# Kernel tuning notes

Hardware: AMD Instinct MI355X
Metric: run time of the kernel (lower is better)

The kernel has to match this reference:

```python
import jax, jax.numpy as jnp
import numpy as np

B, S, D, H = 2, 2048, 2048, 16
NEG = -1e9


def setup_inputs() -> dict:
    key = jax.random.key(0)
    ks = jax.random.split(key, 5)
    x = jax.random.normal(ks[0], (B, S, D), dtype=jnp.float32)
    # additive causal mask: 0 on/below diagonal, -1e9 above
    causal = jnp.triu(jnp.full((S, S), NEG, dtype=jnp.float32), k=1)
    attn_mask = causal[None, None, :, :]  # [1,1,S,S]
    scale = 0.02
    Wq = jax.random.normal(ks[1], (D, D), dtype=jnp.float32) * scale
    Wk = jax.random.normal(ks[2], (D, D), dtype=jnp.float32) * scale
    Wv = jax.random.normal(ks[3], (D, D), dtype=jnp.float32) * scale
    Wo = jax.random.normal(ks[4], (D, D), dtype=jnp.float32) * scale
    return {"x": x, "attn_mask": attn_mask, "Wq": Wq, "Wk": Wk, "Wv": Wv, "Wo": Wo}


def reference(x, attn_mask, Wq, Wk, Wv, Wo):
    b, s, hidden = x.shape
    d = hidden // H
    # torch nn.Linear: y = x @ W.T (no bias since bias=None)
    q = (x @ Wq.T).reshape(b, s, H, d).transpose(0, 2, 1, 3)  # [b,h,s,d]
    k = (x @ Wk.T).reshape(b, s, H, d).transpose(0, 2, 1, 3)
    v = (x @ Wv.T).reshape(b, s, H, d).transpose(0, 2, 1, 3)
    q = q * (1.0 / float(d) ** 0.5)
    att = jnp.einsum("bhqd,bhkd->bhqk", q, k) + attn_mask  # [b,h,s,s]
    att = jax.nn.softmax(att.astype(jnp.float32), axis=-1).astype(x.dtype)
    y = jnp.einsum("bhqk,bhkd->bhqd", att, v)
    y = y.transpose(0, 2, 1, 3).reshape(b, s, hidden)
    return y @ Wo.T
```

## Files before the change

kernel.cpp:

```cpp
#include <hip/hip_runtime.h>
#include <hip/hip_bf16.h>
#include <cstdint>
#include <cstddef>

typedef __bf16 bf16;
typedef __bf16 bf16x8 __attribute__((ext_vector_type(8)));
typedef __bf16 bf16x4 __attribute__((ext_vector_type(4)));
typedef float f32x4 __attribute__((ext_vector_type(4)));

static constexpr int BATCH = 2;
static constexpr int SEQ = 2048;
static constexpr int DMODEL = 2048;
static constexpr int NH = 16;
static constexpr int HD = 128;
static constexpr int MROWS = BATCH * SEQ;

#define GLOBAL_AS(p) ((const __attribute__((address_space(1))) void*)(p))
#define LDS_AS(p)    ((__attribute__((address_space(3))) void*)(p))

__global__ void cvt5_kernel(const float* __restrict__ x,
                            const float* __restrict__ wq, const float* __restrict__ wk,
                            const float* __restrict__ wv, const float* __restrict__ wo,
                            bf16* __restrict__ dst) {
  const int i = blockIdx.x * blockDim.x + threadIdx.x;
  const float* src;
  int local;
  if (i < 2097152) { src = x; local = i; }
  else {
    const int r = i - 2097152;
    const int w = r >> 20;
    local = r & 1048575;
    src = (w == 0) ? wq : (w == 1) ? wk : (w == 2) ? wv : wo;
  }
  float4 f = reinterpret_cast<const float4*>(src)[local];
  bf16x4 o;
  o.x = (bf16)f.x; o.y = (bf16)f.y; o.z = (bf16)f.z; o.w = (bf16)f.w;
  reinterpret_cast<bf16x4*>(dst)[i] = o;
}

enum { MODE_QKV = 0, MODE_OUT = 1 };

template <int MODE>
__global__ __launch_bounds__(256, 4) void gemm_bt(
    const bf16* __restrict__ A, const bf16* __restrict__ W,
    bf16* __restrict__ Oq, bf16* __restrict__ Ok, bf16* __restrict__ Ov,
    float* __restrict__ Oout) {
  constexpr int Kd = DMODEL;
  __shared__ __align__(16) bf16 As[128][64];
  __shared__ __align__(16) bf16 Bs[128][64];
  const int n0 = blockIdx.x * 128;
  const int m0 = blockIdx.y * 128;
  const int tid = threadIdx.x;
  const int wave = tid >> 6;
  const int lane = tid & 63;
  const int quad = lane >> 4;
  const int l16 = lane & 15;
  const int wm = (wave >> 1) * 64;
  const int wn = (wave & 1) * 64;
  const int srow = lane >> 3;
  const int schunk = ((lane & 7) - srow) & 7;

  f32x4 acc[4][4] = {};
  for (int kt = 0; kt < Kd; kt += 64) {
#pragma unroll
    for (int i = 0; i < 4; i++) {
      const int r = wave * 32 + i * 8;
      __builtin_amdgcn_global_load_lds(
          GLOBAL_AS(&A[(size_t)(m0 + r + srow) * Kd + kt + schunk * 8]),
          LDS_AS(&As[r][0]), 16, 0, 0);
      __builtin_amdgcn_global_load_lds(
          GLOBAL_AS(&W[(size_t)(n0 + r + srow) * Kd + kt + schunk * 8]),
          LDS_AS(&Bs[r][0]), 16, 0, 0);
    }
    __syncthreads();
#pragma unroll
    for (int ks = 0; ks < 2; ks++) {
      const int col = (((ks * 4 + quad + l16) & 7)) * 8;
      bf16x8 af[4], bfr[4];
#pragma unroll
      for (int t = 0; t < 4; t++)
        af[t] = *reinterpret_cast<const bf16x8*>(&As[wm + t * 16 + l16][col]);
#pragma unroll
      for (int t = 0; t < 4; t++)
        bfr[t] = *reinterpret_cast<const bf16x8*>(&Bs[wn + t * 16 + l16][col]);
#pragma unroll
      for (int tm = 0; tm < 4; tm++)
#pragma unroll
        for (int tn = 0; tn < 4; tn++)
          acc[tm][tn] = __builtin_amdgcn_mfma_f32_16x16x32_bf16(af[tm], bfr[tn], acc[tm][tn], 0, 0, 0);
    }
    __syncthreads();
  }
#pragma unroll
  for (int tm = 0; tm < 4; tm++) {
#pragma unroll
    for (int tn = 0; tn < 4; tn++) {
      const int row0 = m0 + wm + tm * 16 + quad * 4;
      if constexpr (MODE == MODE_OUT) {
        const int col = n0 + wn + tn * 16 + l16;
#pragma unroll
        for (int j = 0; j < 4; j++)
          Oout[(size_t)(row0 + j) * DMODEL + col] = acc[tm][tn][j];
      } else {
        const int mat = n0 >> 11;
        const int col = (n0 & 2047) + wn + tn * 16 + l16;
        const int h = col >> 7, dd = col & 127;
        if (mat == 2) {
          const int b = row0 >> 11, s = row0 & 2047;
          bf16x4 pk;
#pragma unroll
          for (int j = 0; j < 4; j++) pk[j] = (bf16)acc[tm][tn][j];
          *reinterpret_cast<bf16x4*>(&Ov[((size_t)(b * NH + h) * HD + dd) * SEQ + s]) = pk;
        } else {
          bf16* O = mat ? Ok : Oq;
          const float scale = mat ? 1.0f : 0.08838834764831845f;
#pragma unroll
          for (int j = 0; j < 4; j++) {
            const int row = row0 + j;
            const int b = row >> 11, s = row & 2047;
            O[((size_t)(b * NH + h) * SEQ + s) * HD + dd] = (bf16)(acc[tm][tn][j] * scale);
          }
        }
      }
    }
  }
}

__global__ __launch_bounds__(256, 2) void attn_kernel(
    const bf16* __restrict__ Q, const bf16* __restrict__ K,
    const bf16* __restrict__ Vt, bf16* __restrict__ Y) {
  const int j = blockIdx.x;
  const int bh = blockIdx.y;
  __shared__ __align__(16) char smem[54528];
  auto Ks  = (bf16(*)[128])smem;
  auto Vts = (bf16(*)[64])(smem + 16384);
  auto Ps  = (bf16(*)[16][72])(smem + 32768);
  const int tid = threadIdx.x;
  const int wave = tid >> 6;
  const int lane = tid & 63;
  const int quad = lane >> 4;
  const int l16 = lane & 15;

  const bf16* Kbh = K + (size_t)bh * SEQ * HD;
  const bf16* Vbh = Vt + (size_t)bh * HD * SEQ;
  const int b = bh >> 4, h = bh & 15;

  const int krow = lane >> 4;
  const int vrow = lane >> 3;
  const int vchunk = ((lane & 7) - vrow) & 7;

  for (int pass = 0; pass < 2; ++pass) {
    const int qt = pass ? (31 - j) : j;
    const int q0 = qt * 64;
    const int ntiles = qt + 1;

    const bf16* Qw = Q + ((size_t)bh * SEQ + q0 + wave * 16) * HD;
    bf16x8 qf[4];
#pragma unroll
    for (int kk = 0; kk < 4; kk++)
      qf[kk] = *reinterpret_cast<const bf16x8*>(&Qw[(size_t)l16 * HD + kk * 32 + quad * 8]);

    f32x4 oacc[8] = {};
    float m_i = -3.0e38f, l_i = 0.f;

    for (int t = 0; t < ntiles; ++t) {
      const int kt = t * 64;
#pragma unroll
      for (int i = 0; i < 4; i++) {
        const int rbase = wave * 16 + i * 4;
        const int r = rbase + krow;
        const int c = ((lane & 15) - krow - i * 4) & 15;
        __builtin_amdgcn_global_load_lds(
            GLOBAL_AS(&Kbh[(size_t)(kt + r) * HD + c * 8]), LDS_AS(&Ks[rbase][0]), 16, 0, 0);
      }
#pragma unroll
      for (int i = 0; i < 4; i++) {
        const int rbase = wave * 32 + i * 8;
        const int r = rbase + vrow;
        __builtin_amdgcn_global_load_lds(
            GLOBAL_AS(&Vbh[(size_t)r * SEQ + kt + vchunk * 8]), LDS_AS(&Vts[rbase][0]), 16, 0, 0);
      }
      __syncthreads();

      f32x4 sacc[4] = {};
#pragma unroll
      for (int kk = 0; kk < 4; kk++) {
        const int kcol = (((kk * 4 + quad + l16) & 15)) * 8;
        bf16x8 ka[4];
#pragma unroll
        for (int mt = 0; mt < 4; mt++)
          ka[mt] = *reinterpret_cast<const bf16x8*>(&Ks[mt * 16 + l16][kcol]);
#pragma unroll
        for (int mt = 0; mt < 4; mt++)
          sacc[mt] = __builtin_amdgcn_mfma_f32_16x16x32_bf16(ka[mt], qf[kk], sacc[mt], 0, 0, 0);
      }

      const int qg_loc = wave * 16 + l16;
      float mx = -3.0e38f;
      if (t == ntiles - 1) {
#pragma unroll
        for (int mt = 0; mt < 4; mt++)
#pragma unroll
          for (int jj = 0; jj < 4; jj++) {
            const int kg = mt * 16 + quad * 4 + jj;
            float v = (kg <= qg_loc) ? sacc[mt][jj] : -3.0e38f;
            sacc[mt][jj] = v;
            mx = fmaxf(mx, v);
          }
      } else {
#pragma unroll
        for (int mt = 0; mt < 4; mt++)
#pragma unroll
          for (int jj = 0; jj < 4; jj++) mx = fmaxf(mx, sacc[mt][jj]);
      }
      mx = fmaxf(mx, __shfl_xor(mx, 16));
      mx = fmaxf(mx, __shfl_xor(mx, 32));
      const float mnew = fmaxf(m_i, mx);
      const float alpha = __expf(m_i - mnew);
      m_i = mnew;
      float rs = 0.f;
#pragma unroll
      for (int mt = 0; mt < 4; mt++)
#pragma unroll
        for (int jj = 0; jj < 4; jj++) {
          float p = __expf(sacc[mt][jj] - mnew);
          sacc[mt][jj] = p;
          rs += p;
        }
      rs += __shfl_xor(rs, 16);
      rs += __shfl_xor(rs, 32);
      l_i = l_i * alpha + rs;
#pragma unroll
      for (int mt8 = 0; mt8 < 8; mt8++)
#pragma unroll
        for (int jj = 0; jj < 4; jj++) oacc[mt8][jj] *= alpha;

#pragma unroll
      for (int mt = 0; mt < 4; mt++) {
        bf16x4 pk;
#pragma unroll
        for (int jj = 0; jj < 4; jj++) pk[jj] = (bf16)sacc[mt][jj];
        *reinterpret_cast<bf16x4*>(&Ps[wave][l16][mt * 16 + quad * 4]) = pk;
      }

#pragma unroll
      for (int kk2 = 0; kk2 < 2; kk2++) {
        const int vcol = ((kk2 * 4 + quad + l16) & 7) * 8;
        bf16x8 pb = *reinterpret_cast<const bf16x8*>(&Ps[wave][l16][kk2 * 32 + quad * 8]);
#pragma unroll
        for (int mt8 = 0; mt8 < 8; mt8++) {
          bf16x8 av = *reinterpret_cast<const bf16x8*>(&Vts[mt8 * 16 + l16][vcol]);
          oacc[mt8] = __builtin_amdgcn_mfma_f32_16x16x32_bf16(av, pb, oacc[mt8], 0, 0, 0);
        }
      }
      __syncthreads();
    }

    const float inv = 1.0f / l_i;
    const int qg = q0 + wave * 16 + l16;
#pragma unroll
    for (int mt8 = 0; mt8 < 8; mt8++) {
      bf16x4 pk;
#pragma unroll
      for (int jj = 0; jj < 4; jj++) pk[jj] = (bf16)(oacc[mt8][jj] * inv);
      *reinterpret_cast<bf16x4*>(
          &Y[(size_t)(b * SEQ + qg) * DMODEL + h * HD + mt8 * 16 + quad * 4]) = pk;
    }
  }
}

extern "C" void kernel_launch(void* const* d_in, const int* in_sizes, int n_in,
                              void* d_out, int out_size, void* d_ws, size_t ws_size,
                              hipStream_t stream) {
  const float* x  = (const float*)d_in[0];
  const float* Wq = (const float*)d_in[2];
  const float* Wk = (const float*)d_in[3];
  const float* Wv = (const float*)d_in[4];
  const float* Wo = (const float*)d_in[5];
  float* out = (float*)d_out;

  char* ws = (char*)d_ws;
  bf16* xb  = (bf16*)(ws + 0);
  bf16* Wqb = (bf16*)(ws + 16777216);
  bf16* Wob = (bf16*)(ws + 41943040);
  bf16* Qb  = (bf16*)(ws + 50331648);
  bf16* Kb  = (bf16*)(ws + 67108864);
  bf16* Vtb = (bf16*)(ws + 83886080);
  bf16* Yb  = xb;
  if (ws_size < 100663296) return;

  cvt5_kernel<<<24576, 256, 0, stream>>>(x, Wq, Wk, Wv, Wo, xb);

  gemm_bt<MODE_QKV><<<dim3(48, MROWS / 128), 256, 0, stream>>>(
      xb, Wqb, Qb, Kb, Vtb, nullptr);

  attn_kernel<<<dim3(16, BATCH * NH), 256, 0, stream>>>(Qb, Kb, Vtb, Yb);

  gemm_bt<MODE_OUT><<<dim3(16, MROWS / 128), 256, 0, stream>>>(
      Yb, Wob, nullptr, nullptr, nullptr, out);
}
```

Before: 362.4 us.

## Register-prefetch next K/V tile to overlap global loads with attention compute

```diff
diff --git a/kernel.cpp b/kernel.cpp
--- a/kernel.cpp
+++ b/kernel.cpp
@@ -146,8 +146,16 @@
   const int b = bh >> 4, h = bh & 15;
 
   const int krow = lane >> 4;
+  const int kphys = lane & 15;
   const int vrow = lane >> 3;
-  const int vchunk = ((lane & 7) - vrow) & 7;
+  const int vphys = lane & 7;
+  const int vchunk = (vphys - vrow) & 7;
+  int koff[4], voff[4];
+#pragma unroll
+  for (int i = 0; i < 4; i++) {
+    koff[i] = (wave * 16 + i * 4 + krow) * HD + (((kphys - krow - i * 4) & 15) * 8);
+    voff[i] = (wave * 32 + i * 8 + vrow) * SEQ + vchunk * 8;
+  }
 
   for (int pass = 0; pass < 2; ++pass) {
     const int qt = pass ? (31 - j) : j;
@@ -163,24 +171,30 @@
     f32x4 oacc[8] = {};
     float m_i = -3.0e38f, l_i = 0.f;
 
+    uint4 kpre[4], vpre[4];
+#pragma unroll
+    for (int i = 0; i < 4; i++) {
+      kpre[i] = *reinterpret_cast<const uint4*>(&Kbh[koff[i]]);
+      vpre[i] = *reinterpret_cast<const uint4*>(&Vbh[voff[i]]);
+    }
+
     for (int t = 0; t < ntiles; ++t) {
-      const int kt = t * 64;
+      __syncthreads();
 #pragma unroll
       for (int i = 0; i < 4; i++) {
-        const int rbase = wave * 16 + i * 4;
-        const int r = rbase + krow;
-        const int c = ((lane & 15) - krow - i * 4) & 15;
-        __builtin_amdgcn_global_load_lds(
-            GLOBAL_AS(&Kbh[(size_t)(kt + r) * HD + c * 8]), LDS_AS(&Ks[rbase][0]), 16, 0, 0);
-      }
-#pragma unroll
-      for (int i = 0; i < 4; i++) {
-        const int rbase = wave * 32 + i * 8;
-        const int r = rbase + vrow;
-        __builtin_amdgcn_global_load_lds(
-            GLOBAL_AS(&Vbh[(size_t)r * SEQ + kt + vchunk * 8]), LDS_AS(&Vts[rbase][0]), 16, 0, 0);
+        *reinterpret_cast<uint4*>(&Ks[wave * 16 + i * 4 + krow][kphys * 8]) = kpre[i];
+        *reinterpret_cast<uint4*>(&Vts[wave * 32 + i * 8 + vrow][vphys * 8]) = vpre[i];
       }
       __syncthreads();
+
+      if (t + 1 < ntiles) {
+        const int ktn = (t + 1) * 64;
+#pragma unroll
+        for (int i = 0; i < 4; i++) {
+          kpre[i] = *reinterpret_cast<const uint4*>(&Kbh[(size_t)ktn * HD + koff[i]]);
+          vpre[i] = *reinterpret_cast<const uint4*>(&Vbh[ktn + voff[i]]);
+        }
+      }
 
       f32x4 sacc[4] = {};
 #pragma unroll
@@ -253,7 +267,6 @@
           oacc[mt8] = __builtin_amdgcn_mfma_f32_16x16x32_bf16(av, pb, oacc[mt8], 0, 0, 0);
         }
       }
-      __syncthreads();
     }
 
     const float inv = 1.0f / l_i;
```

Result: slower. 461.2 us (+27.3%).

## Double-buffer K tiles in attention and overlap V loads with QK compute

Applied to the files above, without the earlier changes.

```diff
diff --git a/kernel.cpp b/kernel.cpp
--- a/kernel.cpp
+++ b/kernel.cpp
@@ -17,6 +17,7 @@
 
 #define GLOBAL_AS(p) ((const __attribute__((address_space(1))) void*)(p))
 #define LDS_AS(p)    ((__attribute__((address_space(3))) void*)(p))
+#define WAIT_VMCNT0() __builtin_amdgcn_s_waitcnt(0x0F70)
 
 __global__ void cvt5_kernel(const float* __restrict__ x,
                             const float* __restrict__ wq, const float* __restrict__ wk,
@@ -72,6 +73,7 @@
           GLOBAL_AS(&W[(size_t)(n0 + r + srow) * Kd + kt + schunk * 8]),
           LDS_AS(&Bs[r][0]), 16, 0, 0);
     }
+    WAIT_VMCNT0();
     __syncthreads();
 #pragma unroll
     for (int ks = 0; ks < 2; ks++) {
@@ -131,10 +133,10 @@
     const bf16* __restrict__ Vt, bf16* __restrict__ Y) {
   const int j = blockIdx.x;
   const int bh = blockIdx.y;
-  __shared__ __align__(16) char smem[54528];
-  auto Ks  = (bf16(*)[128])smem;
-  auto Vts = (bf16(*)[64])(smem + 16384);
-  auto Ps  = (bf16(*)[16][72])(smem + 32768);
+  __shared__ __align__(16) char smem[58368];
+  auto Ks  = (bf16(*)[64][128])smem;
+  auto Vts = (bf16(*)[64])(smem + 32768);
+  auto Ps  = (bf16(*)[16][72])(smem + 49152);
   const int tid = threadIdx.x;
   const int wave = tid >> 6;
   const int lane = tid & 63;
@@ -146,8 +148,10 @@
   const int b = bh >> 4, h = bh & 15;
 
   const int krow = lane >> 4;
+  const int kphys = lane & 15;
   const int vrow = lane >> 3;
-  const int vchunk = ((lane & 7) - vrow) & 7;
+  const int vphys = lane & 7;
+  const int vchunk = (vphys - vrow) & 7;
 
   for (int pass = 0; pass < 2; ++pass) {
     const int qt = pass ? (31 - j) : j;
@@ -163,24 +167,29 @@
     f32x4 oacc[8] = {};
     float m_i = -3.0e38f, l_i = 0.f;
 
+    __syncthreads();
+#pragma unroll
+    for (int i = 0; i < 4; i++) {
+      const int rbase = wave * 16 + i * 4;
+      const int c = ((kphys - krow - i * 4) & 15);
+      __builtin_amdgcn_global_load_lds(
+          GLOBAL_AS(&Kbh[(size_t)(rbase + krow) * HD + c * 8]),
+          LDS_AS(&Ks[0][rbase][0]), 16, 0, 0);
+    }
+
     for (int t = 0; t < ntiles; ++t) {
       const int kt = t * 64;
-#pragma unroll
-      for (int i = 0; i < 4; i++) {
-        const int rbase = wave * 16 + i * 4;
-        const int r = rbase + krow;
-        const int c = ((lane & 15) - krow - i * 4) & 15;
-        __builtin_amdgcn_global_load_lds(
-            GLOBAL_AS(&Kbh[(size_t)(kt + r) * HD + c * 8]), LDS_AS(&Ks[rbase][0]), 16, 0, 0);
-      }
+      const int X = t & 1;
+      WAIT_VMCNT0();
+      __syncthreads();
+
 #pragma unroll
       for (int i = 0; i < 4; i++) {
         const int rbase = wave * 32 + i * 8;
-        const int r = rbase + vrow;
         __builtin_amdgcn_global_load_lds(
-            GLOBAL_AS(&Vbh[(size_t)r * SEQ + kt + vchunk * 8]), LDS_AS(&Vts[rbase][0]), 16, 0, 0);
-      }
-      __syncthreads();
+            GLOBAL_AS(&Vbh[(size_t)(rbase + vrow) * SEQ + kt + vchunk * 8]),
+            LDS_AS(&Vts[rbase][0]), 16, 0, 0);
+      }
 
       f32x4 sacc[4] = {};
 #pragma unroll
@@ -189,7 +198,7 @@
         bf16x8 ka[4];
 #pragma unroll
         for (int mt = 0; mt < 4; mt++)
-          ka[mt] = *reinterpret_cast<const bf16x8*>(&Ks[mt * 16 + l16][kcol]);
+          ka[mt] = *reinterpret_cast<const bf16x8*>(&Ks[X][mt * 16 + l16][kcol]);
 #pragma unroll
         for (int mt = 0; mt < 4; mt++)
           sacc[mt] = __builtin_amdgcn_mfma_f32_16x16x32_bf16(ka[mt], qf[kk], sacc[mt], 0, 0, 0);
@@ -243,6 +252,21 @@
         *reinterpret_cast<bf16x4*>(&Ps[wave][l16][mt * 16 + quad * 4]) = pk;
       }
 
+      WAIT_VMCNT0();
+      __syncthreads();
+
+      if (t + 1 < ntiles) {
+        const int ktn = kt + 64;
+#pragma unroll
+        for (int i = 0; i < 4; i++) {
+          const int rbase = wave * 16 + i * 4;
+          const int c = ((kphys - krow - i * 4) & 15);
+          __builtin_amdgcn_global_load_lds(
+              GLOBAL_AS(&Kbh[(size_t)(ktn + rbase + krow) * HD + c * 8]),
+              LDS_AS(&Ks[1 - X][rbase][0]), 16, 0, 0);
+        }
+      }
+
 #pragma unroll
       for (int kk2 = 0; kk2 < 2; kk2++) {
         const int vcol = ((kk2 * 4 + quad + l16) & 7) * 8;
@@ -253,7 +277,6 @@
           oacc[mt8] = __builtin_amdgcn_mfma_f32_16x16x32_bf16(av, pb, oacc[mt8], 0, 0, 0);
         }
       }
-      __syncthreads();
     }
 
     const float inv = 1.0f / l_i;
```

Result: no change. 368.5 us (+1.7%).
